# Performance work log

Hardware: AMD Instinct MI355X
Metric: run time of the kernel (lower is better)

The kernel has to match this reference:

```python
import jax, jax.numpy as jnp
import numpy as np

N, E, D_IN, D_POS, LATENT, C = 50000, 800000, 500, 2, 128, 10
NEG_SLOPE = 0.2

def _glorot(key, shape):
    lim = np.sqrt(6.0 / (shape[0] + shape[1]))
    return jax.random.uniform(key, shape, jnp.float32, -lim, lim)

def setup_inputs() -> dict:
    key = jax.random.key(0)
    ks = jax.random.split(key, 20)
    x = jax.random.normal(ks[0], (N, D_IN), jnp.float32)
    pos = jax.random.uniform(ks[1], (N, D_POS), jnp.float32)
    edge_index = jax.random.randint(ks[2], (2, E), 0, N, jnp.int32)
    edge_attr = jax.random.uniform(ks[3], (E, 1), jnp.float32)
    d0 = D_IN + D_POS
    params = dict(
        W1=_glorot(ks[4], (d0, 512)), b1=jnp.zeros((512,)),
        W2=_glorot(ks[5], (512, 256)), b2=jnp.zeros((256,)),
        W3=_glorot(ks[6], (256, LATENT)), b3=jnp.zeros((LATENT,)),
        Wl=_glorot(ks[7], (LATENT, LATENT)), bl=jnp.zeros((LATENT,)),
        Wr=_glorot(ks[8], (LATENT, LATENT)), br=jnp.zeros((LATENT,)),
        We=_glorot(ks[9], (1, LATENT)),
        att=_glorot(ks[10], (LATENT, 1))[:, 0],
        bg=jnp.zeros((LATENT,)),
        Wd1=_glorot(ks[11], (LATENT, 64)), bd1=jnp.zeros((64,)),
        Wd2=_glorot(ks[12], (64, C)), bd2=jnp.zeros((C,)),
    )
    return dict(x=x, pos=pos, edge_index=edge_index, edge_attr=edge_attr, **params)

def _gatv2(h, src, dst, edge_attr, Wl, bl, Wr, br, We, att, bg):
    n = h.shape[0]
    xl = h @ Wl + bl            # [N, D] source transform
    xr = h @ Wr + br            # [N, D] target transform
    e = edge_attr @ We          # [E, D] edge embedding
    m = xl[src] + xr[dst] + e   # [E, D]
    m = jnp.where(m > 0, m, NEG_SLOPE * m)   # leaky_relu
    s = m @ att                 # [E] attention logits
    smax = jax.lax.stop_gradient(jax.ops.segment_max(s, dst, num_segments=n))
    ex = jnp.exp(s - smax[dst])
    denom = jax.ops.segment_sum(ex, dst, num_segments=n)
    alpha = ex / denom[dst]     # edge softmax over incoming edges
    out = jax.ops.segment_sum(alpha[:, None] * xl[src], dst, num_segments=n)
    return out + bg

def reference(x, pos, edge_index, edge_attr,
              W1, b1, W2, b2, W3, b3,
              Wl, bl, Wr, br, We, att, bg,
              Wd1, bd1, Wd2, bd2):
    xin = jnp.concatenate([x, pos], axis=-1)
    # encoder MLP [-1,512,256,latent], plain_last=True
    h = jax.nn.relu(xin @ W1 + b1)
    h = jax.nn.relu(h @ W2 + b2)
    h = h @ W3 + b3
    # GATv2 spatial channel, then block activation (plain_last=False)
    src, dst = edge_index[0], edge_index[1]
    h = _gatv2(h, src, dst, edge_attr, Wl, bl, Wr, br, We, att, bg)
    z = jax.nn.relu(h)
    # decoder MLP latent->64->C, plain_last, then softmax
    d = jax.nn.relu(z @ Wd1 + bd1)
    logits = d @ Wd2 + bd2
    return jax.nn.softmax(logits, axis=-1)
```

## Files before the change

kernel.cpp:

```cpp
#include <hip/hip_runtime.h>
#include <hip/hip_bf16.h>

#define NEG_SLOPE 0.2f

typedef _Float16 half8   __attribute__((ext_vector_type(8)));
typedef _Float16 half2v  __attribute__((ext_vector_type(2)));
typedef float    float4v __attribute__((ext_vector_type(4)));

__device__ __forceinline__ void gload16(const _Float16* g, _Float16* l)
{
    __builtin_amdgcn_global_load_lds(
        (const __attribute__((address_space(1))) unsigned int*)g,
        (__attribute__((address_space(3))) unsigned int*)l, 16, 0, 0);
}

__global__ __launch_bounds__(256)
void concat_f16_kernel(const float* __restrict__ x, const float* __restrict__ pos,
                       _Float16* __restrict__ A0, int N)
{
    const int total = N * 256;
    for (int i = blockIdx.x * 256 + threadIdx.x; i < total; i += gridDim.x * 256) {
        int node = i >> 8;
        int c2   = (i & 255) * 2;
        float2 v = make_float2(0.f, 0.f);
        if (c2 < 500)       v = *(const float2*)(x + (size_t)node * 500 + c2);
        else if (c2 == 500) v = *(const float2*)(pos + (size_t)node * 2);
        half2v h; h.x = (_Float16)v.x; h.y = (_Float16)v.y;
        *(half2v*)(A0 + (size_t)node * 512 + c2) = h;
    }
}

__global__ void wconv_kernel(const float* __restrict__ W, _Float16* __restrict__ Wt,
                             int K, int Nout, int Kpad)
{
    int total = Nout * Kpad;
    for (int i = blockIdx.x * blockDim.x + threadIdx.x; i < total;
         i += gridDim.x * blockDim.x) {
        int n = i / Kpad, k = i - n * Kpad;
        Wt[i] = (_Float16)((k < K) ? W[(size_t)k * Nout + n] : 0.f);
    }
}

__global__ __launch_bounds__(256)
void wfold_kernel(const float* __restrict__ W3, const float* __restrict__ Wl,
                  const float* __restrict__ Wr, _Float16* __restrict__ Wct)
{
    __shared__ float colv[128];
    const int nn = blockIdx.x;
    const float* Ws = (nn < 128) ? Wl : Wr;
    const int c = nn & 127;
    if (threadIdx.x < 128) colv[threadIdx.x] = Ws[threadIdx.x * 128 + c];
    __syncthreads();
    const int k2 = threadIdx.x;
    const float* wrow = W3 + k2 * 128;
    float s = 0.f;
    #pragma unroll 8
    for (int j = 0; j < 128; ++j) s += wrow[j] * colv[j];
    Wct[nn * 256 + k2] = (_Float16)s;
}

__global__ void bfold_kernel(const float* __restrict__ Wl, const float* __restrict__ Wr,
                             const float* __restrict__ b3, const float* __restrict__ bl,
                             const float* __restrict__ br, float* __restrict__ bcombo)
{
    int nn = threadIdx.x;
    const float* Ws = (nn < 128) ? Wl : Wr;
    int c = nn & 127;
    float s = (nn < 128) ? bl[c] : br[c];
    for (int j = 0; j < 128; ++j) s += b3[j] * Ws[j * 128 + c];
    bcombo[nn] = s;
}

__device__ inline void decode_swz(int b, int nblk, int ny, int& bx, int& by)
{
    int q = nblk >> 3, r = nblk & 7;
    int xcd = b & 7, j = b >> 3;
    int L = (xcd < r ? xcd * (q + 1) : r * (q + 1) + (xcd - r) * q) + j;
    bx = L / ny;
    by = L - bx * ny;
}

template<int WF32, int WF16>
__global__ __launch_bounds__(256)
void gemm_f16_kernel(const _Float16* __restrict__ A, const _Float16* __restrict__ Bt,
                     const float* __restrict__ bias, float* __restrict__ Cf,
                     _Float16* __restrict__ Ch, int M, int N, int K, int ny, int do_relu)
{
    __shared__ __align__(16) _Float16 smem[3][8192];

    int bx, by;
    decode_swz(blockIdx.x, gridDim.x, ny, bx, by);

    const int t    = threadIdx.x;
    const int row0 = bx * 128;
    const int n0   = by * 128;
    const int lane = t & 63;
    const int w    = t >> 6;
    const int wrow = (w >> 1) * 64;
    const int wcol = (w & 1) * 64;
    const int lrow = lane & 15;
    const int lk   = lane >> 4;
    const int sw   = lk ^ ((lrow >> 1) & 3);

    const int rl     = lane >> 2;
    const int lk_log = (lane & 3) ^ ((lane >> 3) & 3);

    int rA0 = row0 + w * 16 + rl;        if (rA0 > M - 1) rA0 = M - 1;
    int rA1 = row0 + (w + 4) * 16 + rl;  if (rA1 > M - 1) rA1 = M - 1;
    int rB0 = n0 + w * 16 + rl;          if (rB0 > N - 1) rB0 = N - 1;
    int rB1 = n0 + (w + 4) * 16 + rl;    if (rB1 > N - 1) rB1 = N - 1;

    const _Float16* gA0 = A  + (size_t)rA0 * K + lk_log * 8;
    const _Float16* gA1 = A  + (size_t)rA1 * K + lk_log * 8;
    const _Float16* gB0 = Bt + (size_t)rB0 * K + lk_log * 8;
    const _Float16* gB1 = Bt + (size_t)rB1 * K + lk_log * 8;

    float4v acc[4][4];
    #pragma unroll
    for (int i = 0; i < 4; ++i)
        #pragma unroll
        for (int j = 0; j < 4; ++j)
            acc[i][j] = (float4v){0.f, 0.f, 0.f, 0.f};

    const int KT = K >> 5;

    auto stage = [&](int kt, int buf) {
        _Float16* sA = &smem[buf][0];
        _Float16* sB = &smem[buf][4096];
        int ko = kt * 32;
        gload16(gA0 + ko, sA + (w    ) * 512);
        gload16(gA1 + ko, sA + (w + 4) * 512);
        gload16(gB0 + ko, sB + (w    ) * 512);
        gload16(gB1 + ko, sB + (w + 4) * 512);
    };

    stage(0, 0);
    if (KT > 1) {
        stage(1, 1);
        asm volatile("s_waitcnt vmcnt(4)" ::: "memory");
    } else {
        asm volatile("s_waitcnt vmcnt(0)" ::: "memory");
    }
    __builtin_amdgcn_sched_barrier(0);
    __builtin_amdgcn_s_barrier();

    for (int kt = 0; kt < KT; ++kt) {
        if (kt + 2 < KT) stage(kt + 2, (kt + 2) % 3);

        const _Float16* bufA = &smem[kt % 3][0];
        const _Float16* bufB = &smem[kt % 3][4096];

        half8 af[4], bf[4];
        #pragma unroll
        for (int mi = 0; mi < 4; ++mi)
            af[mi] = *(const half8*)(bufA + (wrow + mi * 16 + lrow) * 32 + sw * 8);
        #pragma unroll
        for (int ni = 0; ni < 4; ++ni)
            bf[ni] = *(const half8*)(bufB + (wcol + ni * 16 + lrow) * 32 + sw * 8);

        #pragma unroll
        for (int mi = 0; mi < 4; ++mi)
            #pragma unroll
            for (int ni = 0; ni < 4; ++ni)
                acc[mi][ni] = __builtin_amdgcn_mfma_f32_16x16x32_f16(
                    af[mi], bf[ni], acc[mi][ni], 0, 0, 0);

        if (kt + 1 < KT) {
            if (kt + 2 < KT) asm volatile("s_waitcnt vmcnt(4)" ::: "memory");
            else             asm volatile("s_waitcnt vmcnt(0)" ::: "memory");
            __builtin_amdgcn_sched_barrier(0);
            __builtin_amdgcn_s_barrier();
        }
    }

    #pragma unroll
    for (int mi = 0; mi < 4; ++mi) {
        #pragma unroll
        for (int ni = 0; ni < 4; ++ni) {
            #pragma unroll
            for (int r = 0; r < 4; ++r) {
                int row = row0 + wrow + mi * 16 + lk * 4 + r;
                int col = n0 + wcol + ni * 16 + lrow;
                if (row < M && col < N) {
                    float v = acc[mi][ni][r] + bias[col];
                    if (do_relu) v = fmaxf(v, 0.f);
                    if (WF32) Cf[(size_t)row * N + col] = v;
                    if (WF16) Ch[(size_t)row * N + col] = (_Float16)v;
                }
            }
        }
    }
}

__global__ __launch_bounds__(256)
void dec_fused_kernel(const _Float16* __restrict__ zh, const _Float16* __restrict__ Wd1t,
                      const float* __restrict__ bd1, const float* __restrict__ Wd2,
                      const float* __restrict__ bd2, float* __restrict__ out, int n)
{
    __shared__ __align__(16) _Float16 zs[128 * 40];
    __shared__ __align__(16) _Float16 wd1s[64 * 136];
    __shared__ __align__(16) _Float16 dsd[128 * 66];
    __shared__ float wd2s[640];
    __shared__ float bd1s[64];
    __shared__ float bd2s[10];

    const int t    = threadIdx.x;
    const int lane = t & 63;
    const int w    = t >> 6;
    const int wrow = (w >> 1) * 64;
    const int wcol = (w & 1) * 32;
    const int lrow = lane & 15;
    const int lk   = lane >> 4;
    const int node0 = blockIdx.x * 128;

    for (int i = t; i < 64 * 16; i += 256) {
        int r = i >> 4, c8 = i & 15;
        *(half8*)&wd1s[r * 136 + c8 * 8] = *(const half8*)(Wd1t + r * 128 + c8 * 8);
    }
    for (int i = t; i < 640; i += 256) wd2s[i] = Wd2[i];
    if (t < 64) bd1s[t] = bd1[t];
    if (t < 10) bd2s[t] = bd2[t];

    float4v acc[4][2];
    #pragma unroll
    for (int i = 0; i < 4; ++i)
        #pragma unroll
        for (int j = 0; j < 2; ++j)
            acc[i][j] = (float4v){0.f, 0.f, 0.f, 0.f};

    const int zrow = t >> 1;
    const int ch   = t & 1;
    int gz = node0 + zrow; if (gz > n - 1) gz = n - 1;
    const _Float16* zsrc = zh + (size_t)gz * 128 + ch * 16;

    for (int kt = 0; kt < 4; ++kt) {
        __syncthreads();
        *(half8*)&zs[zrow * 40 + ch * 16]     = *(const half8*)(zsrc + kt * 32);
        *(half8*)&zs[zrow * 40 + ch * 16 + 8] = *(const half8*)(zsrc + kt * 32 + 8);
        __syncthreads();

        half8 af[4], bf[2];
        #pragma unroll
        for (int mi = 0; mi < 4; ++mi)
            af[mi] = *(const half8*)&zs[(wrow + mi * 16 + lrow) * 40 + lk * 8];
        #pragma unroll
        for (int ni = 0; ni < 2; ++ni)
            bf[ni] = *(const half8*)&wd1s[(wcol + ni * 16 + lrow) * 136 + kt * 32 + lk * 8];

        #pragma unroll
        for (int mi = 0; mi < 4; ++mi)
            #pragma unroll
            for (int ni = 0; ni < 2; ++ni)
                acc[mi][ni] = __builtin_amdgcn_mfma_f32_16x16x32_f16(
                    af[mi], bf[ni], acc[mi][ni], 0, 0, 0);
    }

    #pragma unroll
    for (int mi = 0; mi < 4; ++mi) {
        #pragma unroll
        for (int ni = 0; ni < 2; ++ni) {
            #pragma unroll
            for (int r = 0; r < 4; ++r) {
                int rr = wrow + mi * 16 + lk * 4 + r;
                int cc = wcol + ni * 16 + lrow;
                float v = fmaxf(acc[mi][ni][r] + bd1s[cc], 0.f);
                dsd[rr * 66 + cc] = (_Float16)v;
            }
        }
    }
    __syncthreads();

    if (t < 128) {
        int node = node0 + t;
        if (node < n) {
            float lg[10];
            #pragma unroll
            for (int c = 0; c < 10; ++c) lg[c] = bd2s[c];
            #pragma unroll
            for (int k8 = 0; k8 < 8; ++k8) {
                half8 dv = *(const half8*)&dsd[t * 66 + k8 * 8];
                #pragma unroll
                for (int j = 0; j < 8; ++j) {
                    float dj = (float)dv[j];
                    #pragma unroll
                    for (int c = 0; c < 10; ++c)
                        lg[c] += dj * wd2s[(k8 * 8 + j) * 10 + c];
                }
            }
            float mx = lg[0];
            #pragma unroll
            for (int c = 1; c < 10; ++c) mx = fmaxf(mx, lg[c]);
            float ssum = 0.f;
            #pragma unroll
            for (int c = 0; c < 10; ++c) { lg[c] = expf(lg[c] - mx); ssum += lg[c]; }
            float inv = 1.f / ssum;
            #pragma unroll
            for (int c = 0; c < 10; ++c)
                out[(size_t)node * 10 + c] = lg[c] * inv;
        }
    }
}

__global__ void count_edges_kernel(const int* __restrict__ dst, int* cnt, int E)
{
    int e = blockIdx.x * blockDim.x + threadIdx.x;
    if (e < E) atomicAdd(&cnt[dst[e]], 1);
}

__global__ __launch_bounds__(256)
void block_sum_kernel(const int* __restrict__ cnt, int* __restrict__ bsum, int n)
{
    __shared__ int sh[256];
    int t = threadIdx.x;
    int i = blockIdx.x * 256 + t;
    sh[t] = (i < n) ? cnt[i] : 0;
    __syncthreads();
    #pragma unroll
    for (int off = 128; off > 0; off >>= 1) {
        if (t < off) sh[t] += sh[t + off];
        __syncthreads();
    }
    if (t == 0) bsum[blockIdx.x] = sh[0];
}

__global__ __launch_bounds__(256)
void scan_bsum_kernel(int* __restrict__ bsum, int* __restrict__ row_start, int nb, int n)
{
    __shared__ int sh[256];
    int t = threadIdx.x;
    int v = (t < nb) ? bsum[t] : 0;
    sh[t] = v;
    __syncthreads();
    #pragma unroll
    for (int off = 1; off < 256; off <<= 1) {
        int xv = (t >= off) ? sh[t - off] : 0;
        __syncthreads();
        sh[t] += xv;
        __syncthreads();
    }
    if (t < nb) bsum[t] = sh[t] - v;
    if (t == 255) row_start[n] = sh[255];
}

__global__ __launch_bounds__(256)
void scan_final_kernel(const int* __restrict__ cnt, const int* __restrict__ boff,
                       int* __restrict__ row_start, int* __restrict__ cursor, int n)
{
    __shared__ int sh[256];
    int t = threadIdx.x;
    int i = blockIdx.x * 256 + t;
    int v = (i < n) ? cnt[i] : 0;
    sh[t] = v;
    __syncthreads();
    #pragma unroll
    for (int off = 1; off < 256; off <<= 1) {
        int xv = (t >= off) ? sh[t - off] : 0;
        __syncthreads();
        sh[t] += xv;
        __syncthreads();
    }
    if (i < n) {
        int ex = boff[blockIdx.x] + sh[t] - v;
        row_start[i] = ex;
        cursor[i]    = ex;
    }
}

__global__ void scatter_edges_kernel(const int* __restrict__ dst, const int* __restrict__ src,
                                     const float* __restrict__ ea, int* cursor,
                                     int2* __restrict__ recs, int E)
{
    int e = blockIdx.x * blockDim.x + threadIdx.x;
    if (e < E) {
        int p = atomicAdd(&cursor[dst[e]], 1);
        recs[p] = make_int2(src[e], __float_as_int(ea[e]));
    }
}

__global__ __launch_bounds__(256)
void gat_aggregate_kernel(const _Float16* __restrict__ xlr, const int2* __restrict__ recs,
                          const float* __restrict__ We, const float* __restrict__ att,
                          const float* __restrict__ bg, const int* __restrict__ row_start,
                          _Float16* __restrict__ z, int n)
{
    const int wave = threadIdx.x >> 6;
    const int lane = threadIdx.x & 63;
    const int node = blockIdx.x * 4 + wave;
    if (node >= n) return;

    const int g  = lane >> 4;
    const int sl = lane & 15;
    const int d0 = sl * 8;

    half2v at_h[4], we_h[4], xr_h[4];
    {
        float4 a0 = *(const float4*)(att + d0);
        float4 a1 = *(const float4*)(att + d0 + 4);
        float4 w0 = *(const float4*)(We + d0);
        float4 w1 = *(const float4*)(We + d0 + 4);
        at_h[0] = (half2v){(_Float16)a0.x, (_Float16)a0.y};
        at_h[1] = (half2v){(_Float16)a0.z, (_Float16)a0.w};
        at_h[2] = (half2v){(_Float16)a1.x, (_Float16)a1.y};
        at_h[3] = (half2v){(_Float16)a1.z, (_Float16)a1.w};
        we_h[0] = (half2v){(_Float16)w0.x, (_Float16)w0.y};
        we_h[1] = (half2v){(_Float16)w0.z, (_Float16)w0.w};
        we_h[2] = (half2v){(_Float16)w1.x, (_Float16)w1.y};
        we_h[3] = (half2v){(_Float16)w1.z, (_Float16)w1.w};
        half8 xh = *(const half8*)(xlr + (size_t)node * 256 + 128 + d0);
        #pragma unroll
        for (int q = 0; q < 4; ++q)
            xr_h[q] = (half2v){xh[2 * q], xh[2 * q + 1]};
    }
    const half2v slope2 = (half2v){(_Float16)NEG_SLOPE, (_Float16)NEG_SLOPE};

    const int beg = row_start[node];
    const int end = row_start[node + 1];

    float m_run = -INFINITY;
    float l_run = 0.f;
    float acc[8];
    #pragma unroll
    for (int j = 0; j < 8; ++j) acc[j] = 0.f;

    for (int idx = beg + g; idx < end; idx += 4) {
        int2 rec = recs[idx];
        _Float16 eh = (_Float16)__int_as_float(rec.y);
        half2v e2 = (half2v){eh, eh};
        half8 xh = *(const half8*)(xlr + (size_t)rec.x * 256 + d0);

        float part = 0.f;
        #pragma unroll
        for (int q = 0; q < 4; ++q) {
            half2v xq = (half2v){xh[2 * q], xh[2 * q + 1]};
            half2v mq = xq + (e2 * we_h[q] + xr_h[q]);
            half2v lq = __builtin_elementwise_max(mq, mq * slope2);
#if __has_builtin(__builtin_amdgcn_fdot2)
            part = __builtin_amdgcn_fdot2(lq, at_h[q], part, false);
#else
            part += (float)lq.x * (float)at_h[q].x + (float)lq.y * (float)at_h[q].y;
#endif
        }
        part += __shfl_xor(part, 1);
        part += __shfl_xor(part, 2);
        part += __shfl_xor(part, 4);
        part += __shfl_xor(part, 8);

        if (part <= m_run + 8.f) {
            float p = __expf(part - m_run);
            l_run += p;
            #pragma unroll
            for (int j = 0; j < 8; ++j) acc[j] += p * (float)xh[j];
        } else {
            float sc = __expf(m_run - part);
            l_run = l_run * sc + 1.f;
            #pragma unroll
            for (int j = 0; j < 8; ++j) acc[j] = acc[j] * sc + (float)xh[j];
            m_run = part;
        }
    }

    #pragma unroll
    for (int off = 16; off <= 32; off <<= 1) {
        float m_o = __shfl_xor(m_run, off);
        float l_o = __shfl_xor(l_run, off);
        float mn  = fmaxf(m_run, m_o);
        float sa  = (m_run == mn) ? 1.f : __expf(m_run - mn);
        float sb  = (m_o   == mn) ? 1.f : __expf(m_o - mn);
        l_run = l_run * sa + l_o * sb;
        #pragma unroll
        for (int j = 0; j < 8; ++j) {
            float a_o = __shfl_xor(acc[j], off);
            acc[j] = acc[j] * sa + a_o * sb;
        }
        m_run = mn;
    }

    if (g == 0) {
        float inv = (l_run > 0.f) ? 1.f / l_run : 0.f;
        const float* bgp = bg + d0;
        half8 o;
        #pragma unroll
        for (int j = 0; j < 8; ++j) {
            float v = fmaxf(acc[j] * inv + bgp[j], 0.f);
            o[j] = (_Float16)v;
        }
        *(half8*)(z + (size_t)node * 128 + d0) = o;
    }
}

extern "C" void kernel_launch(void* const* d_in, const int* in_sizes, int n_in,
                              void* d_out, int out_size, void* d_ws, size_t ws_size,
                              hipStream_t stream)
{
    const float* x    = (const float*)d_in[0];
    const float* pos  = (const float*)d_in[1];
    const int*   ei   = (const int*)d_in[2];
    const float* ea   = (const float*)d_in[3];
    const float* W1   = (const float*)d_in[4];
    const float* b1   = (const float*)d_in[5];
    const float* W2   = (const float*)d_in[6];
    const float* b2   = (const float*)d_in[7];
    const float* W3   = (const float*)d_in[8];
    const float* b3   = (const float*)d_in[9];
    const float* Wl   = (const float*)d_in[10];
    const float* bl   = (const float*)d_in[11];
    const float* Wr   = (const float*)d_in[12];
    const float* br   = (const float*)d_in[13];
    const float* We   = (const float*)d_in[14];
    const float* att  = (const float*)d_in[15];
    const float* bg   = (const float*)d_in[16];
    const float* Wd1  = (const float*)d_in[17];
    const float* bd1  = (const float*)d_in[18];
    const float* Wd2  = (const float*)d_in[19];
    const float* bd2  = (const float*)d_in[20];
    float* out = (float*)d_out;

    const int N = in_sizes[0] / 500;
    const int E = in_sizes[2] / 2;

    char* base = (char*)d_ws;
    const size_t szR = (size_t)N * 512 * 2;
    _Float16* A0h = (_Float16*)(base);
    _Float16* h2h = (_Float16*)(base);
    _Float16* zh  = (_Float16*)(base + (size_t)N * 384 * 2);
    char* r1 = base + szR;
    _Float16* h1h = (_Float16*)(r1);
    _Float16* xlr = (_Float16*)(r1);
    char* r2 = base + 2 * szR;
    _Float16* W1t   = (_Float16*)(r2);
    _Float16* W2t   = W1t  + 512 * 512;
    _Float16* Wct   = W2t  + 256 * 512;
    _Float16* Wd1t  = Wct  + 256 * 256;
    float*    bcombo = (float*)(Wd1t + 64 * 128);
    int* cnt       = (int*)(r2 + 2 * 1024 * 1024);
    int* row_start = cnt + N;
    int* bsum      = row_start + N + 1;
    int2* recs     = (int2*)(r2 + 3 * 1024 * 1024);

    const int* srcArr = ei;
    const int* dstArr = ei + E;
    const int gx = (N + 127) / 128;
    const int nb = (N + 255) / 256;

    concat_f16_kernel<<<2048, 256, 0, stream>>>(x, pos, A0h, N);
    wconv_kernel<<<1024, 256, 0, stream>>>(W1,  W1t,  502, 512, 512);
    wconv_kernel<<<512,  256, 0, stream>>>(W2,  W2t,  512, 256, 512);
    wconv_kernel<<<32,   256, 0, stream>>>(Wd1, Wd1t, 128, 64,  128);
    wfold_kernel<<<256, 256, 0, stream>>>(W3, Wl, Wr, Wct);
    bfold_kernel<<<1, 256, 0, stream>>>(Wl, Wr, b3, bl, br, bcombo);

    hipMemsetAsync(cnt, 0, (size_t)N * sizeof(int), stream);
    count_edges_kernel<<<(E + 255) / 256, 256, 0, stream>>>(dstArr, cnt, E);
    block_sum_kernel<<<nb, 256, 0, stream>>>(cnt, bsum, N);
    scan_bsum_kernel<<<1, 256, 0, stream>>>(bsum, row_start, nb, N);
    scan_final_kernel<<<nb, 256, 0, stream>>>(cnt, bsum, row_start, cnt, N);
    scatter_edges_kernel<<<(E + 255) / 256, 256, 0, stream>>>(dstArr, srcArr, ea, cnt, recs, E);

    gemm_f16_kernel<0,1><<<gx * 4, 256, 0, stream>>>(A0h, W1t, b1, nullptr, h1h, N, 512, 512, 4, 1);
    gemm_f16_kernel<0,1><<<gx * 2, 256, 0, stream>>>(h1h, W2t, b2, nullptr, h2h, N, 256, 512, 2, 1);
    gemm_f16_kernel<0,1><<<gx * 2, 256, 0, stream>>>(h2h, Wct, bcombo, nullptr, xlr, N, 256, 256, 2, 0);

    gat_aggregate_kernel<<<(N + 3) / 4, 256, 0, stream>>>(xlr, recs, We, att, bg,
                                                          row_start, zh, N);

    dec_fused_kernel<<<gx, 256, 0, stream>>>(zh, Wd1t, bd1, Wd2, bd2, out, N);
}
```

Measured before the change: 331.0 us.

## Merge prep kernels into one launch and overlap edge scatter with first GEMM

Folds the input concat, weight conversions, weight/bias folding and edge counting into a single block-indexed prep kernel, cutting several launches and their tail gaps. The edge scatter is appended as extra blocks to the first GEMM launch, so its atomics and writes run alongside the GEMM tiles. This trades launch overhead and serialization for heterogeneous blocks contending for CUs. The GEMM's LDS allocation may also lower occupancy for the scatter blocks.

```diff
diff --git a/kernel.cpp b/kernel.cpp
--- a/kernel.cpp
+++ b/kernel.cpp
@@ -15,60 +15,73 @@
 }
 
 __global__ __launch_bounds__(256)
-void concat_f16_kernel(const float* __restrict__ x, const float* __restrict__ pos,
-                       _Float16* __restrict__ A0, int N)
-{
-    const int total = N * 256;
-    for (int i = blockIdx.x * 256 + threadIdx.x; i < total; i += gridDim.x * 256) {
-        int node = i >> 8;
-        int c2   = (i & 255) * 2;
-        float2 v = make_float2(0.f, 0.f);
-        if (c2 < 500)       v = *(const float2*)(x + (size_t)node * 500 + c2);
-        else if (c2 == 500) v = *(const float2*)(pos + (size_t)node * 2);
-        half2v h; h.x = (_Float16)v.x; h.y = (_Float16)v.y;
-        *(half2v*)(A0 + (size_t)node * 512 + c2) = h;
-    }
-}
-
-__global__ void wconv_kernel(const float* __restrict__ W, _Float16* __restrict__ Wt,
-                             int K, int Nout, int Kpad)
-{
-    int total = Nout * Kpad;
-    for (int i = blockIdx.x * blockDim.x + threadIdx.x; i < total;
-         i += gridDim.x * blockDim.x) {
-        int n = i / Kpad, k = i - n * Kpad;
-        Wt[i] = (_Float16)((k < K) ? W[(size_t)k * Nout + n] : 0.f);
-    }
-}
-
-__global__ __launch_bounds__(256)
-void wfold_kernel(const float* __restrict__ W3, const float* __restrict__ Wl,
-                  const float* __restrict__ Wr, _Float16* __restrict__ Wct)
-{
-    __shared__ float colv[128];
-    const int nn = blockIdx.x;
-    const float* Ws = (nn < 128) ? Wl : Wr;
-    const int c = nn & 127;
-    if (threadIdx.x < 128) colv[threadIdx.x] = Ws[threadIdx.x * 128 + c];
-    __syncthreads();
-    const int k2 = threadIdx.x;
-    const float* wrow = W3 + k2 * 128;
-    float s = 0.f;
-    #pragma unroll 8
-    for (int j = 0; j < 128; ++j) s += wrow[j] * colv[j];
-    Wct[nn * 256 + k2] = (_Float16)s;
-}
-
-__global__ void bfold_kernel(const float* __restrict__ Wl, const float* __restrict__ Wr,
-                             const float* __restrict__ b3, const float* __restrict__ bl,
-                             const float* __restrict__ br, float* __restrict__ bcombo)
-{
-    int nn = threadIdx.x;
-    const float* Ws = (nn < 128) ? Wl : Wr;
-    int c = nn & 127;
-    float s = (nn < 128) ? bl[c] : br[c];
-    for (int j = 0; j < 128; ++j) s += b3[j] * Ws[j * 128 + c];
-    bcombo[nn] = s;
+void prep_mega_kernel(const float* __restrict__ x, const float* __restrict__ pos,
+                      _Float16* __restrict__ A0,
+                      const float* __restrict__ W1, _Float16* __restrict__ W1t,
+                      const float* __restrict__ W2, _Float16* __restrict__ W2t,
+                      const float* __restrict__ Wd1, _Float16* __restrict__ Wd1t,
+                      const float* __restrict__ W3, const float* __restrict__ Wl,
+                      const float* __restrict__ Wr, _Float16* __restrict__ Wct,
+                      const float* __restrict__ b3, const float* __restrict__ bl,
+                      const float* __restrict__ br, float* __restrict__ bcombo,
+                      const int* __restrict__ dstA, int* __restrict__ cnt,
+                      int N, int E)
+{
+    const int b = blockIdx.x;
+    const int t = threadIdx.x;
+
+    if (b < 2048) {
+        const int total = N * 256;
+        for (int i = b * 256 + t; i < total; i += 2048 * 256) {
+            int node = i >> 8;
+            int c2   = (i & 255) * 2;
+            float2 v = make_float2(0.f, 0.f);
+            if (c2 < 500)       v = *(const float2*)(x + (size_t)node * 500 + c2);
+            else if (c2 == 500) v = *(const float2*)(pos + (size_t)node * 2);
+            half2v h; h.x = (_Float16)v.x; h.y = (_Float16)v.y;
+            *(half2v*)(A0 + (size_t)node * 512 + c2) = h;
+        }
+    } else if (b < 2304) {
+        int bb = b - 2048;
+        for (int i = bb * 256 + t; i < 512 * 512; i += 256 * 256) {
+            int n = i >> 9, k = i & 511;
+            W1t[i] = (_Float16)((k < 502) ? W1[(size_t)k * 512 + n] : 0.f);
+        }
+    } else if (b < 2432) {
+        int bb = b - 2304;
+        for (int i = bb * 256 + t; i < 256 * 512; i += 128 * 256) {
+            int n = i >> 9, k = i & 511;
+            W2t[i] = (_Float16)W2[(size_t)k * 256 + n];
+        }
+    } else if (b < 2440) {
+        int bb = b - 2432;
+        for (int i = bb * 256 + t; i < 64 * 128; i += 8 * 256) {
+            int n = i >> 7, k = i & 127;
+            Wd1t[i] = (_Float16)Wd1[(size_t)k * 64 + n];
+        }
+    } else if (b < 2696) {
+        __shared__ float colv[128];
+        int nn = b - 2440;
+        const float* Ws = (nn < 128) ? Wl : Wr;
+        int c = nn & 127;
+        if (t < 128) colv[t] = Ws[t * 128 + c];
+        __syncthreads();
+        const float* wrow = W3 + t * 128;
+        float s = 0.f;
+        #pragma unroll 8
+        for (int j = 0; j < 128; ++j) s += wrow[j] * colv[j];
+        Wct[nn * 256 + t] = (_Float16)s;
+    } else if (b == 2696) {
+        int nn = t;
+        const float* Ws = (nn < 128) ? Wl : Wr;
+        int c = nn & 127;
+        float s = (nn < 128) ? bl[c] : br[c];
+        for (int j = 0; j < 128; ++j) s += b3[j] * Ws[j * 128 + c];
+        bcombo[nn] = s;
+    } else {
+        int e = (b - 2697) * 256 + t;
+        if (e < E) atomicAdd(&cnt[dstA[e]], 1);
+    }
 }
 
 __device__ inline void decode_swz(int b, int nblk, int ny, int& bx, int& by)
@@ -80,16 +93,28 @@
     by = L - bx * ny;
 }
 
-template<int WF32, int WF16>
+template<int WF32, int WF16, int SCAT>
 __global__ __launch_bounds__(256)
 void gemm_f16_kernel(const _Float16* __restrict__ A, const _Float16* __restrict__ Bt,
                      const float* __restrict__ bias, float* __restrict__ Cf,
-                     _Float16* __restrict__ Ch, int M, int N, int K, int ny, int do_relu)
+                     _Float16* __restrict__ Ch, int M, int N, int K, int ny, int do_relu,
+                     const int* __restrict__ s_dst, const int* __restrict__ s_src,
+                     const float* __restrict__ s_ea, int* __restrict__ s_cursor,
+                     int2* __restrict__ s_recs, int s_E, int gemm_nblk)
 {
     __shared__ __align__(16) _Float16 smem[3][8192];
 
+    if (SCAT && (int)blockIdx.x >= gemm_nblk) {
+        int e = ((int)blockIdx.x - gemm_nblk) * 256 + threadIdx.x;
+        if (e < s_E) {
+            int p = atomicAdd(&s_cursor[s_dst[e]], 1);
+            s_recs[p] = make_int2(s_src[e], __float_as_int(s_ea[e]));
+        }
+        return;
+    }
+
     int bx, by;
-    decode_swz(blockIdx.x, gridDim.x, ny, bx, by);
+    decode_swz(blockIdx.x, gemm_nblk, ny, bx, by);
 
     const int t    = threadIdx.x;
     const int row0 = bx * 128;
@@ -301,12 +326,6 @@
     }
 }
 
-__global__ void count_edges_kernel(const int* __restrict__ dst, int* cnt, int E)
-{
-    int e = blockIdx.x * blockDim.x + threadIdx.x;
-    if (e < E) atomicAdd(&cnt[dst[e]], 1);
-}
-
 __global__ __launch_bounds__(256)
 void block_sum_kernel(const int* __restrict__ cnt, int* __restrict__ bsum, int n)
 {
@@ -363,17 +382,6 @@
         int ex = boff[blockIdx.x] + sh[t] - v;
         row_start[i] = ex;
         cursor[i]    = ex;
-    }
-}
-
-__global__ void scatter_edges_kernel(const int* __restrict__ dst, const int* __restrict__ src,
-                                     const float* __restrict__ ea, int* cursor,
-                                     int2* __restrict__ recs, int E)
-{
-    int e = blockIdx.x * blockDim.x + threadIdx.x;
-    if (e < E) {
-        int p = atomicAdd(&cursor[dst[e]], 1);
-        recs[p] = make_int2(src[e], __float_as_int(ea[e]));
     }
 }
 
@@ -541,24 +549,26 @@
     const int* dstArr = ei + E;
     const int gx = (N + 127) / 128;
     const int nb = (N + 255) / 256;
-
-    concat_f16_kernel<<<2048, 256, 0, stream>>>(x, pos, A0h, N);
-    wconv_kernel<<<1024, 256, 0, stream>>>(W1,  W1t,  502, 512, 512);
-    wconv_kernel<<<512,  256, 0, stream>>>(W2,  W2t,  512, 256, 512);
-    wconv_kernel<<<32,   256, 0, stream>>>(Wd1, Wd1t, 128, 64,  128);
-    wfold_kernel<<<256, 256, 0, stream>>>(W3, Wl, Wr, Wct);
-    bfold_kernel<<<1, 256, 0, stream>>>(Wl, Wr, b3, bl, br, bcombo);
+    const int scat_blocks = (E + 255) / 256;
 
     hipMemsetAsync(cnt, 0, (size_t)N * sizeof(int), stream);
-    count_edges_kernel<<<(E + 255) / 256, 256, 0, stream>>>(dstArr, cnt, E);
+    prep_mega_kernel<<<2697 + scat_blocks, 256, 0, stream>>>(
+        x, pos, A0h, W1, W1t, W2, W2t, Wd1, Wd1t,
+        W3, Wl, Wr, Wct, b3, bl, br, bcombo, dstArr, cnt, N, E);
+
     block_sum_kernel<<<nb, 256, 0, stream>>>(cnt, bsum, N);
     scan_bsum_kernel<<<1, 256, 0, stream>>>(bsum, row_start, nb, N);
     scan_final_kernel<<<nb, 256, 0, stream>>>(cnt, bsum, row_start, cnt, N);
-    scatter_edges_kernel<<<(E + 255) / 256, 256, 0, stream>>>(dstArr, srcArr, ea, cnt, recs, E);
-
-    gemm_f16_kernel<0,1><<<gx * 4, 256, 0, stream>>>(A0h, W1t, b1, nullptr, h1h, N, 512, 512, 4, 1);
-    gemm_f16_kernel<0,1><<<gx * 2, 256, 0, stream>>>(h1h, W2t, b2, nullptr, h2h, N, 256, 512, 2, 1);
-    gemm_f16_kernel<0,1><<<gx * 2, 256, 0, stream>>>(h2h, Wct, bcombo, nullptr, xlr, N, 256, 256, 2, 0);
+
+    gemm_f16_kernel<0,1,1><<<gx * 4 + scat_blocks, 256, 0, stream>>>(
+        A0h, W1t, b1, nullptr, h1h, N, 512, 512, 4, 1,
+        dstArr, srcArr, ea, cnt, recs, E, gx * 4);
+    gemm_f16_kernel<0,1,0><<<gx * 2, 256, 0, stream>>>(
+        h1h, W2t, b2, nullptr, h2h, N, 256, 512, 2, 1,
+        nullptr, nullptr, nullptr, nullptr, nullptr, 0, gx * 2);
+    gemm_f16_kernel<0,1,0><<<gx * 2, 256, 0, stream>>>(
+        h2h, Wct, bcombo, nullptr, xlr, N, 256, 256, 2, 0,
+        nullptr, nullptr, nullptr, nullptr, nullptr, 0, gx * 2);
 
     gat_aggregate_kernel<<<(N + 3) / 4, 256, 0, stream>>>(xlr, recs, We, att, bg,
                                                           row_start, zh, N);
```

New measurement: 310.8 us. -6.1%, faster.
